# Optimization experiments

Hardware: AMD Instinct MI355X
Metric: run time of the kernel (lower is better)

Reference implementation:

```python
import jax, jax.numpy as jnp
import numpy as np

B, T, D, H = 4, 2048, 1024, 16
HD = D // H


def setup_inputs() -> dict:
    key = jax.random.key(0)
    ks = jax.random.split(key, 9)
    s = 1.0 / np.sqrt(D)
    return {
        "x": jax.random.normal(ks[0], (B, T, D), dtype=jnp.float32),
        "Wq": jax.random.normal(ks[1], (D, D), dtype=jnp.float32) * s,
        "bq": jnp.zeros((D,), dtype=jnp.float32),
        "Wk": jax.random.normal(ks[2], (D, D), dtype=jnp.float32) * s,
        "bk": jnp.zeros((D,), dtype=jnp.float32),
        "Wv": jax.random.normal(ks[3], (D, D), dtype=jnp.float32) * s,
        "bv": jnp.zeros((D,), dtype=jnp.float32),
        "Wo": jax.random.normal(ks[4], (D, D), dtype=jnp.float32) * s,
        "bo": jnp.zeros((D,), dtype=jnp.float32),
    }


def reference(x, Wq, bq, Wk, bk, Wv, bv, Wo, bo):
    b, t, c = x.shape
    h, hd = H, HD
    scale = hd ** -0.5
    # projections: [B,T,C] -> [B,H,T,hd]
    q = (x @ Wq.T + bq).reshape(b, t, h, hd).transpose(0, 2, 1, 3)
    k = (x @ Wk.T + bk).reshape(b, t, h, hd).transpose(0, 2, 1, 3)
    v = (x @ Wv.T + bv).reshape(b, t, h, hd).transpose(0, 2, 1, 3)
    # scores [B,H,T,T], causal mask (no kv cache path, T > 1)
    attn = jnp.einsum("bhqd,bhkd->bhqk", q, k) * scale
    causal = jnp.triu(jnp.ones((t, t), dtype=bool), k=1)
    attn = jnp.where(causal, -jnp.inf, attn)
    attn = jax.nn.softmax(attn, axis=-1)
    out = jnp.einsum("bhqk,bhkd->bhqd", attn, v)
    out = out.transpose(0, 2, 1, 3).reshape(b, t, c)
    return (out @ Wo.T + bo, k, v)
```

## Files before the change

### kernel.cpp

```cpp
#include <hip/hip_runtime.h>
#include <hip/hip_bf16.h>
#include <cstdint>


typedef short bf16x8 __attribute__((ext_vector_type(8)));
typedef float f32x4 __attribute__((ext_vector_type(4)));

#define GLDS16(g, l)                                                          \
  __builtin_amdgcn_global_load_lds(                                           \
      (const __attribute__((address_space(1))) void*)(g),                     \
      (__attribute__((address_space(3))) void*)(l), 16, 0, 0)

static __device__ __forceinline__ short f2b(float f) {
  union { float f; unsigned u; } x; x.f = f;
  unsigned r = (x.u + 0x7FFFu + ((x.u >> 16) & 1u)) >> 16;
  return (short)r;
}

static __device__ __forceinline__ unsigned cvtpk2(float a, float b) {
  unsigned r;
  asm("v_cvt_pk_bf16_f32 %0, %1, %2" : "=v"(r) : "v"(a), "v"(b));
  return r;
}

__global__ void cvt_f32_bf16(const float* __restrict__ src, short* __restrict__ dst, int n4) {
  int i = blockIdx.x * blockDim.x + threadIdx.x;
  if (i < n4) {
    float4 v = ((const float4*)src)[i];
    short4 o; o.x = f2b(v.x); o.y = f2b(v.y); o.z = f2b(v.z); o.w = f2b(v.w);
    ((short4*)dst)[i] = o;
  }
}

__global__ void cvt_w4(const float* __restrict__ a, const float* __restrict__ b,
                       const float* __restrict__ c, const float* __restrict__ d,
                       short* __restrict__ dst) {
  int i = blockIdx.x * blockDim.x + threadIdx.x;
  int sel = i >> 18, j = i & 262143;
  const float* src = sel == 0 ? a : sel == 1 ? b : sel == 2 ? c : d;
  float4 v = ((const float4*)src)[j];
  short4 o; o.x = f2b(v.x); o.y = f2b(v.y); o.z = f2b(v.z); o.w = f2b(v.w);
  ((short4*)dst)[i] = o;
}

template <int MODE>
__global__ __launch_bounds__(256) void gemm_bt(
    const short* __restrict__ A, const short* __restrict__ Bm,
    const float* __restrict__ bias,
    float* __restrict__ out_f, short* __restrict__ out_b) {
  __shared__ short As[128 * 32];
  __shared__ short Bs[128 * 32];
  const int t = threadIdx.x;
  const int lane = t & 63;
  const int w = t >> 6;
  const int wm = w >> 1, wn = w & 1;
  const int quad = lane >> 4, l15 = lane & 15;
  const int bm = blockIdx.y, bn = blockIdx.x;

  f32x4 acc[4][4];
  for (int i = 0; i < 4; i++)
    for (int j = 0; j < 4; j++) acc[i][j] = (f32x4){0.f, 0.f, 0.f, 0.f};

  const int c0 = t, c1 = t + 256;
  const int r0 = c0 >> 2, cc0 = c0 & 3;
  const int r1 = c1 >> 2, cc1 = c1 & 3;
  const short* Abase = A + (size_t)bm * 128 * 1024;
  const short* Bbase = Bm + (size_t)bn * 128 * 1024;

  for (int kk = 0; kk < 1024; kk += 32) {
    __syncthreads();
    GLDS16(Abase + (size_t)r0 * 1024 + kk + cc0 * 8, &As[c0 * 8]);
    GLDS16(Abase + (size_t)r1 * 1024 + kk + cc1 * 8, &As[c1 * 8]);
    GLDS16(Bbase + (size_t)r0 * 1024 + kk + cc0 * 8, &Bs[c0 * 8]);
    GLDS16(Bbase + (size_t)r1 * 1024 + kk + cc1 * 8, &Bs[c1 * 8]);
    __syncthreads();
    bf16x8 af[4], bfr[4];
    for (int mt = 0; mt < 4; mt++)
      af[mt] = *(const bf16x8*)(As + (wm * 64 + mt * 16 + l15) * 32 + quad * 8);
    for (int nt = 0; nt < 4; nt++)
      bfr[nt] = *(const bf16x8*)(Bs + (wn * 64 + nt * 16 + l15) * 32 + quad * 8);
    for (int mt = 0; mt < 4; mt++)
      for (int nt = 0; nt < 4; nt++)
        acc[mt][nt] = __builtin_amdgcn_mfma_f32_16x16x32_bf16(af[mt], bfr[nt], acc[mt][nt], 0, 0, 0);
  }

  for (int mt = 0; mt < 4; mt++) {
    const int row_base = bm * 128 + wm * 64 + mt * 16 + quad * 4;
    for (int nt = 0; nt < 4; nt++) {
      const int col = bn * 128 + wn * 64 + nt * 16 + l15;
      const float bb = bias[col];
      for (int r = 0; r < 4; r++) {
        const int row = row_base + r;
        const float v = acc[mt][nt][r] + bb;
        if (MODE == 3) {
          out_f[(size_t)row * 1024 + col] = v;
        } else {
          const int b = row >> 11, tt = row & 2047;
          const int h = col >> 6, hi = col & 63;
          const size_t idx = (((size_t)(b * 16 + h)) * 2048 + tt) * 64 + hi;
          if (MODE == 0) {
            out_b[idx] = f2b(v);
          } else if (MODE == 1) {
            out_f[idx] = v; out_b[idx] = f2b(v);
          } else {
            out_f[idx] = v;
            out_b[(((size_t)(b * 16 + h)) * 64 + hi) * 2048 + tt] = f2b(v);
          }
        }
      }
    }
  }
}

__global__ __launch_bounds__(256) void gemm_qkv(
    const short* __restrict__ A,
    const short* __restrict__ W0, const short* __restrict__ W1, const short* __restrict__ W2,
    const float* __restrict__ b0, const float* __restrict__ b1, const float* __restrict__ b2,
    float* __restrict__ kf, float* __restrict__ vf,
    short* __restrict__ qbo, short* __restrict__ kbo, short* __restrict__ vtbo) {
  __shared__ short As[128 * 32];
  __shared__ short Bs[128 * 32];
  const int t = threadIdx.x;
  const int lane = t & 63;
  const int w = t >> 6;
  const int wm = w >> 1, wn = w & 1;
  const int quad = lane >> 4, l15 = lane & 15;
  const int bm = blockIdx.y;
  const int sel = blockIdx.x >> 3, bn = blockIdx.x & 7;
  const short* Bm = sel == 0 ? W0 : (sel == 1 ? W1 : W2);
  const float* bias = sel == 0 ? b0 : (sel == 1 ? b1 : b2);

  f32x4 acc[4][4];
  for (int i = 0; i < 4; i++)
    for (int j = 0; j < 4; j++) acc[i][j] = (f32x4){0.f, 0.f, 0.f, 0.f};

  const int c0 = t, c1 = t + 256;
  const int r0 = c0 >> 2, cc0 = c0 & 3;
  const int r1 = c1 >> 2, cc1 = c1 & 3;
  const short* Abase = A + (size_t)bm * 128 * 1024;
  const short* Bbase = Bm + (size_t)bn * 128 * 1024;

  for (int kk = 0; kk < 1024; kk += 32) {
    __syncthreads();
    GLDS16(Abase + (size_t)r0 * 1024 + kk + cc0 * 8, &As[c0 * 8]);
    GLDS16(Abase + (size_t)r1 * 1024 + kk + cc1 * 8, &As[c1 * 8]);
    GLDS16(Bbase + (size_t)r0 * 1024 + kk + cc0 * 8, &Bs[c0 * 8]);
    GLDS16(Bbase + (size_t)r1 * 1024 + kk + cc1 * 8, &Bs[c1 * 8]);
    __syncthreads();
    bf16x8 af[4], bfr[4];
    for (int mt = 0; mt < 4; mt++)
      af[mt] = *(const bf16x8*)(As + (wm * 64 + mt * 16 + l15) * 32 + quad * 8);
    for (int nt = 0; nt < 4; nt++)
      bfr[nt] = *(const bf16x8*)(Bs + (wn * 64 + nt * 16 + l15) * 32 + quad * 8);
    for (int mt = 0; mt < 4; mt++)
      for (int nt = 0; nt < 4; nt++)
        acc[mt][nt] = __builtin_amdgcn_mfma_f32_16x16x32_bf16(af[mt], bfr[nt], acc[mt][nt], 0, 0, 0);
  }

  for (int mt = 0; mt < 4; mt++) {
    const int row_base = bm * 128 + wm * 64 + mt * 16 + quad * 4;
    for (int nt = 0; nt < 4; nt++) {
      const int col = bn * 128 + wn * 64 + nt * 16 + l15;
      const float bb = bias[col];
      for (int r = 0; r < 4; r++) {
        const int row = row_base + r;
        const float v = acc[mt][nt][r] + bb;
        const int b = row >> 11, tt = row & 2047;
        const int h = col >> 6, hi = col & 63;
        const size_t idx = (((size_t)(b * 16 + h)) * 2048 + tt) * 64 + hi;
        if (sel == 0) {
          qbo[idx] = f2b(v);
        } else if (sel == 1) {
          kf[idx] = v; kbo[idx] = f2b(v);
        } else {
          vf[idx] = v;
          vtbo[(((size_t)(b * 16 + h)) * 64 + hi) * 2048 + tt] = f2b(v);
        }
      }
    }
  }
}

__global__ __launch_bounds__(256, 4) void attn_fwd(
    const short* __restrict__ Qb, const short* __restrict__ Kb,
    const short* __restrict__ VTb, short* __restrict__ Ob) {
  __shared__ short Ks[128 * 64];
  __shared__ short VTs[64 * 128];
  const int t = threadIdx.x;
  const int w = t >> 6;
  const int lane = t & 63;
  const int quad = lane >> 4, l15 = lane & 15;

  const int L = blockIdx.x + (blockIdx.y << 4);
  const int work = ((L & 7) << 7) + (L >> 3);
  const int bh = work >> 4;
  const int base = work & 15;
  const int b = bh >> 4, h = bh & 15;

  const short* Qh = Qb + (size_t)bh * 2048 * 64;
  const short* Kh = Kb + (size_t)bh * 2048 * 64;
  const short* VTh = VTb + (size_t)bh * 64 * 2048;
  unsigned* Pd = (unsigned*)Ks + w * 1024;
  const int swz = (l15 & 7) << 2;
  const float sscale = 0.125f * 1.4426950408889634f;

  for (int s = 0; s < 2; ++s) {
    const int qt = s ? (31 - base) : base;
    const int q0 = qt * 64 + w * 16;
    const bf16x8 qf0 = *(const bf16x8*)(Qh + (q0 + l15) * 64 + quad * 8);
    const bf16x8 qf1 = *(const bf16x8*)(Qh + (q0 + l15) * 64 + quad * 8 + 32);

    float m_q = -1e30f, l_q = 0.f;
    f32x4 o[4];
    for (int nt = 0; nt < 4; nt++) o[nt] = (f32x4){0.f, 0.f, 0.f, 0.f};
    const int ntile = (qt >> 1) + 1;

    for (int jt = 0; jt < ntile; ++jt) {
      const int j0 = jt << 7;
      __syncthreads();
      for (int rr = 0; rr < 4; rr++) {
        const int c = rr * 256 + t;
        const int row = c >> 3, colL = c & 7;
        const int colg = colL ^ (row & 7);
        GLDS16(Kh + (size_t)(j0 + row) * 64 + colg * 8, &Ks[c * 8]);
      }
      for (int rr = 0; rr < 4; rr++) {
        const int c = rr * 256 + t;
        const int row = c >> 4, colL = c & 15;
        const int colg = colL ^ (row & 7);
        GLDS16(VTh + (size_t)row * 2048 + j0 + colg * 8, &VTs[c * 8]);
      }
      __syncthreads();

      float sv[8][4];
      for (int si = 0; si < 8; ++si) {
        const int r = si * 16 + l15;
        bf16x8 kf0 = *(const bf16x8*)&Ks[(r * 8 + (quad ^ (r & 7))) * 8];
        bf16x8 kf1 = *(const bf16x8*)&Ks[(r * 8 + ((quad ^ 4) ^ (r & 7))) * 8];
        f32x4 z = (f32x4){0.f, 0.f, 0.f, 0.f};
        z = __builtin_amdgcn_mfma_f32_16x16x32_bf16(kf0, qf0, z, 0, 0, 0);
        z = __builtin_amdgcn_mfma_f32_16x16x32_bf16(kf1, qf1, z, 0, 0, 0);
        for (int r4 = 0; r4 < 4; r4++) sv[si][r4] = z[r4];
      }
      if (jt == ntile - 1) {
        const int qg = q0 + l15;
        for (int si = 0; si < 8; si++) {
          const int kbase = j0 + si * 16 + quad * 4;
          for (int r4 = 0; r4 < 4; r4++)
            if (kbase + r4 > qg) sv[si][r4] = -1e30f;
        }
      }
      float vmax = fmaxf(fmaxf(sv[0][0], sv[0][1]), fmaxf(sv[0][2], sv[0][3]));
      for (int si = 1; si < 8; si++) {
        float m2 = fmaxf(fmaxf(sv[si][0], sv[si][1]), fmaxf(sv[si][2], sv[si][3]));
        vmax = fmaxf(vmax, m2);
      }
      vmax = fmaxf(vmax, __shfl_xor(vmax, 16));
      vmax = fmaxf(vmax, __shfl_xor(vmax, 32));
      const float mn = fmaxf(m_q, vmax);
      if (__any(vmax > m_q)) {
        const float alpha = __builtin_amdgcn_exp2f((m_q - mn) * sscale);
        l_q *= alpha;
        float ar[4];
        for (int r4 = 0; r4 < 4; r4++) ar[r4] = __shfl(alpha, quad * 4 + r4);
        for (int nt = 0; nt < 4; nt++)
          for (int r4 = 0; r4 < 4; r4++) o[nt][r4] *= ar[r4];
      }
      m_q = mn;
      __syncthreads();

      const float negmns = -mn * sscale;
      float ssum = 0.f;
      for (int si = 0; si < 8; si++) {
        float p0 = __builtin_amdgcn_exp2f(fmaf(sv[si][0], sscale, negmns));
        float p1 = __builtin_amdgcn_exp2f(fmaf(sv[si][1], sscale, negmns));
        float p2 = __builtin_amdgcn_exp2f(fmaf(sv[si][2], sscale, negmns));
        float p3 = __builtin_amdgcn_exp2f(fmaf(sv[si][3], sscale, negmns));
        ssum += (p0 + p1) + (p2 + p3);
        uint2 pk; pk.x = cvtpk2(p0, p1); pk.y = cvtpk2(p2, p3);
        *(uint2*)(Pd + l15 * 64 + ((si * 8 + quad * 2) ^ swz)) = pk;
      }
      ssum += __shfl_xor(ssum, 16);
      ssum += __shfl_xor(ssum, 32);
      l_q += ssum;

      for (int kc = 0; kc < 4; kc++) {
        bf16x8 pf = *(const bf16x8*)(Pd + l15 * 64 + ((kc * 16 + quad * 4) ^ swz));
        for (int nt = 0; nt < 4; nt++) {
          const int rv = nt * 16 + l15;
          bf16x8 vf = *(const bf16x8*)&VTs[(rv * 16 + ((kc * 4 + quad) ^ (rv & 7))) * 8];
          o[nt] = __builtin_amdgcn_mfma_f32_16x16x32_bf16(pf, vf, o[nt], 0, 0, 0);
        }
      }
    }

    float lr[4], ri[4];
    for (int r4 = 0; r4 < 4; r4++) lr[r4] = __shfl(l_q, quad * 4 + r4);
    for (int r4 = 0; r4 < 4; r4++) ri[r4] = __builtin_amdgcn_rcpf(lr[r4]);
    for (int nt = 0; nt < 4; nt++) {
      const int col = h * 64 + nt * 16 + l15;
      for (int r4 = 0; r4 < 4; r4++) {
        const int q = q0 + quad * 4 + r4;
        Ob[((size_t)b * 2048 + q) * 1024 + col] = f2b(o[nt][r4] * ri[r4]);
      }
    }
  }
}

extern "C" void kernel_launch(void* const* d_in, const int* in_sizes, int n_in,
                              void* d_out, int out_size, void* d_ws, size_t ws_size,
                              hipStream_t stream) {
  const float* x  = (const float*)d_in[0];
  const float* Wq = (const float*)d_in[1];
  const float* bq = (const float*)d_in[2];
  const float* Wk = (const float*)d_in[3];
  const float* bk = (const float*)d_in[4];
  const float* Wv = (const float*)d_in[5];
  const float* bv = (const float*)d_in[6];
  const float* Wo = (const float*)d_in[7];
  const float* bo = (const float*)d_in[8];

  float* out   = (float*)d_out;
  float* k_out = out + (size_t)8388608;
  float* v_out = out + (size_t)16777216;

  short* ws  = (short*)d_ws;
  short* xb   = ws;
  short* wqb  = ws + 8388608;
  short* wkb  = ws + 9437184;
  short* wvb  = ws + 10485760;
  short* wob  = ws + 11534336;
  short* qb   = ws + 12582912;
  short* kb   = ws + 20971520;
  short* vtb  = ws + 29360128;
  short* attb = ws + 37748736;

  cvt_f32_bf16<<<8192, 256, 0, stream>>>(x, xb, 2097152);
  cvt_w4<<<4096, 256, 0, stream>>>(Wq, Wk, Wv, Wo, wqb);

  gemm_qkv<<<dim3(24, 64), 256, 0, stream>>>(
      xb, wqb, wkb, wvb, bq, bk, bv, k_out, v_out, qb, kb, vtb);

  attn_fwd<<<dim3(16, 64), 256, 0, stream>>>(qb, kb, vtb, attb);

  gemm_bt<3><<<dim3(8, 64), 256, 0, stream>>>(attb, wob, bo, out, nullptr);
}
```

Measured before the change: 356.3 us.

## Triple-buffer GEMM K-loop with async LDS loads and transpose V output via LDS

```diff
diff --git a/kernel.cpp b/kernel.cpp
--- a/kernel.cpp
+++ b/kernel.cpp
@@ -43,74 +43,25 @@
   ((short4*)dst)[i] = o;
 }
 
-template <int MODE>
-__global__ __launch_bounds__(256) void gemm_bt(
-    const short* __restrict__ A, const short* __restrict__ Bm,
-    const float* __restrict__ bias,
-    float* __restrict__ out_f, short* __restrict__ out_b) {
-  __shared__ short As[128 * 32];
-  __shared__ short Bs[128 * 32];
-  const int t = threadIdx.x;
-  const int lane = t & 63;
-  const int w = t >> 6;
-  const int wm = w >> 1, wn = w & 1;
-  const int quad = lane >> 4, l15 = lane & 15;
-  const int bm = blockIdx.y, bn = blockIdx.x;
-
-  f32x4 acc[4][4];
-  for (int i = 0; i < 4; i++)
-    for (int j = 0; j < 4; j++) acc[i][j] = (f32x4){0.f, 0.f, 0.f, 0.f};
-
-  const int c0 = t, c1 = t + 256;
-  const int r0 = c0 >> 2, cc0 = c0 & 3;
-  const int r1 = c1 >> 2, cc1 = c1 & 3;
-  const short* Abase = A + (size_t)bm * 128 * 1024;
-  const short* Bbase = Bm + (size_t)bn * 128 * 1024;
-
-  for (int kk = 0; kk < 1024; kk += 32) {
-    __syncthreads();
-    GLDS16(Abase + (size_t)r0 * 1024 + kk + cc0 * 8, &As[c0 * 8]);
-    GLDS16(Abase + (size_t)r1 * 1024 + kk + cc1 * 8, &As[c1 * 8]);
-    GLDS16(Bbase + (size_t)r0 * 1024 + kk + cc0 * 8, &Bs[c0 * 8]);
-    GLDS16(Bbase + (size_t)r1 * 1024 + kk + cc1 * 8, &Bs[c1 * 8]);
-    __syncthreads();
-    bf16x8 af[4], bfr[4];
-    for (int mt = 0; mt < 4; mt++)
-      af[mt] = *(const bf16x8*)(As + (wm * 64 + mt * 16 + l15) * 32 + quad * 8);
-    for (int nt = 0; nt < 4; nt++)
-      bfr[nt] = *(const bf16x8*)(Bs + (wn * 64 + nt * 16 + l15) * 32 + quad * 8);
-    for (int mt = 0; mt < 4; mt++)
-      for (int nt = 0; nt < 4; nt++)
-        acc[mt][nt] = __builtin_amdgcn_mfma_f32_16x16x32_bf16(af[mt], bfr[nt], acc[mt][nt], 0, 0, 0);
-  }
-
-  for (int mt = 0; mt < 4; mt++) {
-    const int row_base = bm * 128 + wm * 64 + mt * 16 + quad * 4;
-    for (int nt = 0; nt < 4; nt++) {
-      const int col = bn * 128 + wn * 64 + nt * 16 + l15;
-      const float bb = bias[col];
-      for (int r = 0; r < 4; r++) {
-        const int row = row_base + r;
-        const float v = acc[mt][nt][r] + bb;
-        if (MODE == 3) {
-          out_f[(size_t)row * 1024 + col] = v;
-        } else {
-          const int b = row >> 11, tt = row & 2047;
-          const int h = col >> 6, hi = col & 63;
-          const size_t idx = (((size_t)(b * 16 + h)) * 2048 + tt) * 64 + hi;
-          if (MODE == 0) {
-            out_b[idx] = f2b(v);
-          } else if (MODE == 1) {
-            out_f[idx] = v; out_b[idx] = f2b(v);
-          } else {
-            out_f[idx] = v;
-            out_b[(((size_t)(b * 16 + h)) * 64 + hi) * 2048 + tt] = f2b(v);
-          }
-        }
-      }
-    }
-  }
-}
+#define PIPE_STEP(BUF)                                                        \
+  {                                                                          \
+    asm volatile("s_waitcnt vmcnt(4) lgkmcnt(0)" ::: "memory");              \
+    __builtin_amdgcn_s_barrier();                                            \
+    __builtin_amdgcn_sched_barrier(0);                                       \
+    stage((((BUF) + 2) % 3), (tile + 2) * 32);                               \
+    compute(BUF);                                                            \
+    ++tile;                                                                  \
+  }
+
+#define PIPE_TAIL()                                                          \
+  asm volatile("s_waitcnt vmcnt(4) lgkmcnt(0)" ::: "memory");                \
+  __builtin_amdgcn_s_barrier();                                              \
+  __builtin_amdgcn_sched_barrier(0);                                         \
+  compute(0);                                                   \
+  asm volatile("s_waitcnt vmcnt(0) lgkmcnt(0)" ::: "memory");                \
+  __builtin_amdgcn_s_barrier();                                              \
+  __builtin_amdgcn_sched_barrier(0);                                         \
+  compute(1);
 
 __global__ __launch_bounds__(256) void gemm_qkv(
     const short* __restrict__ A,
@@ -118,8 +69,7 @@
     const float* __restrict__ b0, const float* __restrict__ b1, const float* __restrict__ b2,
     float* __restrict__ kf, float* __restrict__ vf,
     short* __restrict__ qbo, short* __restrict__ kbo, short* __restrict__ vtbo) {
-  __shared__ short As[128 * 32];
-  __shared__ short Bs[128 * 32];
+  __shared__ short SM[24576];
   const int t = threadIdx.x;
   const int lane = t & 63;
   const int w = t >> 6;
@@ -140,22 +90,140 @@
   const short* Abase = A + (size_t)bm * 128 * 1024;
   const short* Bbase = Bm + (size_t)bn * 128 * 1024;
 
-  for (int kk = 0; kk < 1024; kk += 32) {
-    __syncthreads();
-    GLDS16(Abase + (size_t)r0 * 1024 + kk + cc0 * 8, &As[c0 * 8]);
-    GLDS16(Abase + (size_t)r1 * 1024 + kk + cc1 * 8, &As[c1 * 8]);
-    GLDS16(Bbase + (size_t)r0 * 1024 + kk + cc0 * 8, &Bs[c0 * 8]);
-    GLDS16(Bbase + (size_t)r1 * 1024 + kk + cc1 * 8, &Bs[c1 * 8]);
-    __syncthreads();
+  auto stage = [&](int buf, int kk) {
+    short* A_ = SM + buf * 4096;
+    short* B_ = SM + 12288 + buf * 4096;
+    GLDS16(Abase + (size_t)r0 * 1024 + kk + cc0 * 8, A_ + c0 * 8);
+    GLDS16(Abase + (size_t)r1 * 1024 + kk + cc1 * 8, A_ + c1 * 8);
+    GLDS16(Bbase + (size_t)r0 * 1024 + kk + cc0 * 8, B_ + c0 * 8);
+    GLDS16(Bbase + (size_t)r1 * 1024 + kk + cc1 * 8, B_ + c1 * 8);
+  };
+  auto compute = [&](int buf) {
+    const short* A_ = SM + buf * 4096;
+    const short* B_ = SM + 12288 + buf * 4096;
     bf16x8 af[4], bfr[4];
     for (int mt = 0; mt < 4; mt++)
-      af[mt] = *(const bf16x8*)(As + (wm * 64 + mt * 16 + l15) * 32 + quad * 8);
+      af[mt] = *(const bf16x8*)(A_ + (wm * 64 + mt * 16 + l15) * 32 + quad * 8);
     for (int nt = 0; nt < 4; nt++)
-      bfr[nt] = *(const bf16x8*)(Bs + (wn * 64 + nt * 16 + l15) * 32 + quad * 8);
+      bfr[nt] = *(const bf16x8*)(B_ + (wn * 64 + nt * 16 + l15) * 32 + quad * 8);
     for (int mt = 0; mt < 4; mt++)
       for (int nt = 0; nt < 4; nt++)
         acc[mt][nt] = __builtin_amdgcn_mfma_f32_16x16x32_bf16(af[mt], bfr[nt], acc[mt][nt], 0, 0, 0);
-  }
+  };
+
+  stage(0, 0);
+  stage(1, 32);
+  int tile = 0;
+  for (int ii = 0; ii < 10; ++ii) {
+    PIPE_STEP(0) PIPE_STEP(1) PIPE_STEP(2)
+  }
+  PIPE_TAIL()
+
+  if (sel != 2) {
+    for (int mt = 0; mt < 4; mt++) {
+      const int row_base = bm * 128 + wm * 64 + mt * 16 + quad * 4;
+      for (int nt = 0; nt < 4; nt++) {
+        const int col = bn * 128 + wn * 64 + nt * 16 + l15;
+        const float bb = bias[col];
+        for (int r = 0; r < 4; r++) {
+          const int row = row_base + r;
+          const float v = acc[mt][nt][r] + bb;
+          const int b = row >> 11, tt = row & 2047;
+          const int h = col >> 6, hi = col & 63;
+          const size_t idx = (((size_t)(b * 16 + h)) * 2048 + tt) * 64 + hi;
+          if (sel == 0) {
+            qbo[idx] = f2b(v);
+          } else {
+            kf[idx] = v; kbo[idx] = f2b(v);
+          }
+        }
+      }
+    }
+  } else {
+    short* Tr = SM;
+    __syncthreads();
+    for (int mt = 0; mt < 4; mt++) {
+      const int rowb = wm * 64 + mt * 16 + quad * 4;
+      const int growb = bm * 128 + rowb;
+      const int b_ = growb >> 11;
+      for (int nt = 0; nt < 4; nt++) {
+        const int colL = wn * 64 + nt * 16 + l15;
+        const int col = bn * 128 + colL;
+        const float bb = bias[col];
+        const int h_ = col >> 6, hi_ = col & 63;
+        short4 pk;
+        for (int r = 0; r < 4; r++) {
+          const float v = acc[mt][nt][r] + bb;
+          const int tt = (growb + r) & 2047;
+          vf[(((size_t)(b_ * 16 + h_)) * 2048 + tt) * 64 + hi_] = v;
+          ((short*)&pk)[r] = f2b(v);
+        }
+        *(short4*)&Tr[colL * 136 + rowb] = pk;
+      }
+    }
+    __syncthreads();
+    const int c = t & 127, half = t >> 7;
+    const int gcol = bn * 128 + c;
+    const int h_ = gcol >> 6, hi_ = gcol & 63;
+    for (int j = 0; j < 8; j++) {
+      const int chunk = half * 8 + j;
+      const int row0 = bm * 128 + chunk * 8;
+      const int b_ = row0 >> 11, tt = row0 & 2047;
+      bf16x8 val = *(const bf16x8*)&Tr[c * 136 + chunk * 8];
+      *(bf16x8*)&vtbo[(((size_t)(b_ * 16 + h_)) * 64 + hi_) * 2048 + tt] = val;
+    }
+  }
+}
+
+__global__ __launch_bounds__(256) void gemm_o(
+    const short* __restrict__ A, const short* __restrict__ Bm,
+    const float* __restrict__ bias, float* __restrict__ out_f) {
+  __shared__ short SM[24576];
+  const int t = threadIdx.x;
+  const int lane = t & 63;
+  const int w = t >> 6;
+  const int wm = w >> 1, wn = w & 1;
+  const int quad = lane >> 4, l15 = lane & 15;
+  const int bm = blockIdx.y, bn = blockIdx.x;
+
+  f32x4 acc[4][4];
+  for (int i = 0; i < 4; i++)
+    for (int j = 0; j < 4; j++) acc[i][j] = (f32x4){0.f, 0.f, 0.f, 0.f};
+
+  const int c0 = t, c1 = t + 256;
+  const int r0 = c0 >> 2, cc0 = c0 & 3;
+  const int r1 = c1 >> 2, cc1 = c1 & 3;
+  const short* Abase = A + (size_t)bm * 128 * 1024;
+  const short* Bbase = Bm + (size_t)bn * 128 * 1024;
+
+  auto stage = [&](int buf, int kk) {
+    short* A_ = SM + buf * 4096;
+    short* B_ = SM + 12288 + buf * 4096;
+    GLDS16(Abase + (size_t)r0 * 1024 + kk + cc0 * 8, A_ + c0 * 8);
+    GLDS16(Abase + (size_t)r1 * 1024 + kk + cc1 * 8, A_ + c1 * 8);
+    GLDS16(Bbase + (size_t)r0 * 1024 + kk + cc0 * 8, B_ + c0 * 8);
+    GLDS16(Bbase + (size_t)r1 * 1024 + kk + cc1 * 8, B_ + c1 * 8);
+  };
+  auto compute = [&](int buf) {
+    const short* A_ = SM + buf * 4096;
+    const short* B_ = SM + 12288 + buf * 4096;
+    bf16x8 af[4], bfr[4];
+    for (int mt = 0; mt < 4; mt++)
+      af[mt] = *(const bf16x8*)(A_ + (wm * 64 + mt * 16 + l15) * 32 + quad * 8);
+    for (int nt = 0; nt < 4; nt++)
+      bfr[nt] = *(const bf16x8*)(B_ + (wn * 64 + nt * 16 + l15) * 32 + quad * 8);
+    for (int mt = 0; mt < 4; mt++)
+      for (int nt = 0; nt < 4; nt++)
+        acc[mt][nt] = __builtin_amdgcn_mfma_f32_16x16x32_bf16(af[mt], bfr[nt], acc[mt][nt], 0, 0, 0);
+  };
+
+  stage(0, 0);
+  stage(1, 32);
+  int tile = 0;
+  for (int ii = 0; ii < 10; ++ii) {
+    PIPE_STEP(0) PIPE_STEP(1) PIPE_STEP(2)
+  }
+  PIPE_TAIL()
 
   for (int mt = 0; mt < 4; mt++) {
     const int row_base = bm * 128 + wm * 64 + mt * 16 + quad * 4;
@@ -164,18 +232,7 @@
       const float bb = bias[col];
       for (int r = 0; r < 4; r++) {
         const int row = row_base + r;
-        const float v = acc[mt][nt][r] + bb;
-        const int b = row >> 11, tt = row & 2047;
-        const int h = col >> 6, hi = col & 63;
-        const size_t idx = (((size_t)(b * 16 + h)) * 2048 + tt) * 64 + hi;
-        if (sel == 0) {
-          qbo[idx] = f2b(v);
-        } else if (sel == 1) {
-          kf[idx] = v; kbo[idx] = f2b(v);
-        } else {
-          vf[idx] = v;
-          vtbo[(((size_t)(b * 16 + h)) * 64 + hi) * 2048 + tt] = f2b(v);
-        }
+        out_f[(size_t)row * 1024 + col] = acc[mt][nt][r] + bb;
       }
     }
   }
@@ -343,5 +400,5 @@
 
   attn_fwd<<<dim3(16, 64), 256, 0, stream>>>(qb, kb, vtb, attb);
 
-  gemm_bt<3><<<dim3(8, 64), 256, 0, stream>>>(attb, wob, bo, out, nullptr);
-}
+  gemm_o<<<dim3(8, 64), 256, 0, stream>>>(attb, wob, bo, out);
+}
```

Measured after the change: 328.6 us. 1.08x faster.
